# Kernel optimization log

Measured on AMD Instinct MI355X. Metric: run time of the kernel, lower is better.

Reference implementation:

```python
import jax, jax.numpy as jnp
import numpy as np

B, S, D, E, H, TOPK = 4, 2048, 1024, 32, 128, 4

def setup_inputs() -> dict:
    key = jax.random.key(0)
    k1, k2, k3, k4 = jax.random.split(key, 4)
    x = jax.random.normal(k1, (B, S, D), jnp.float32)
    expert_sel = jax.random.normal(k2, (E, D), jnp.float32) * (D ** -0.5)
    keys = jax.random.normal(k3, (E, D, H), jnp.float32) * (D ** -0.5)
    values = jax.random.normal(k4, (E, H, D), jnp.float32) * (H ** -0.5)
    return {"x": x, "expert_sel": expert_sel, "keys": keys, "values": values, "n_heads": TOPK}

def reference(x, expert_sel, keys, values, n_heads):
    # x: [B,S,D]; expert_sel: [E,D]; keys: [E,D,H]; values: [E,H,D]
    Bv, Sv, Dv = x.shape
    Ev = keys.shape[0]
    xf = x.reshape(-1, Dv)                                  # [N,D]
    N = xf.shape[0]
    gate = jax.nn.sigmoid(xf @ expert_sel.T)                # [N,E] sigmoid gating (sigma-MoE)
    vals, idx = jax.lax.top_k(gate, n_heads)                # [N,k] selected experts + gate weights
    # dense per-token-per-expert gate weights; zero for non-selected experts
    g = jnp.zeros((N, Ev), x.dtype).at[jnp.arange(N)[:, None], idx].set(vals)  # [N,E]
    # grouped expert FFN, expressed densely over the (small) expert axis:
    # out = sum_e g[n,e] * relu(x @ keys[e]) @ values[e]
    h = jax.nn.relu(jnp.einsum('nd,edh->enh', xf, keys))    # [E,N,H]
    out = jnp.einsum('enh,ehd->nd', h * g.T[:, :, None], values)  # [N,D]
    return out.reshape(Bv, Sv, Dv)
```

## Files before the change

### kernel.cpp

```cpp
#include <hip/hip_runtime.h>
#include <hip/hip_bf16.h>

#define NTOK 8192
#define DDIM 1024
#define NEXP 32
#define HDIM 128
#define TOPK 4

typedef __attribute__((ext_vector_type(8))) short bf16x8;
typedef __attribute__((ext_vector_type(4))) float f32x4;

typedef unsigned int uint_g __attribute__((address_space(1)));
typedef unsigned int uint_l __attribute__((address_space(3)));

__device__ __forceinline__ void async_cp16(const void* g, void* l) {
    __builtin_amdgcn_global_load_lds((const uint_g*)g, (uint_l*)l, 16, 0, 0);
}

__device__ inline unsigned short f2bf(float f) {
    unsigned int u = __builtin_bit_cast(unsigned int, f);
    unsigned int r = (u + 0x7fffu + ((u >> 16) & 1u)) >> 16;
    return (unsigned short)r;
}
__device__ inline float bf2f(unsigned short s) {
    unsigned int u = ((unsigned int)s) << 16;
    return __builtin_bit_cast(float, u);
}

__global__ __launch_bounds__(256) void prep_weights(
    const float* __restrict__ x,
    const float* __restrict__ keys, const float* __restrict__ values,
    unsigned short* __restrict__ Kb, unsigned short* __restrict__ Vb,
    unsigned short* __restrict__ Xb)
{
    int idx = blockIdx.x * 256 + threadIdx.x;
    unsigned short o[8];
    if (idx < NEXP * 128 * 128) {
        int n = idx & 127, k0 = (idx >> 7) & 127, e = idx >> 14;
        const float* s = keys + ((size_t)e * DDIM + k0 * 8) * HDIM + n;
        #pragma unroll
        for (int j = 0; j < 8; ++j) o[j] = f2bf(s[(size_t)j * HDIM]);
        *(uint4*)&Kb[(size_t)idx * 8] = *(uint4*)o;
    } else if (idx < 2 * NEXP * 128 * 128) {
        idx -= NEXP * 128 * 128;
        int n = idx & 1023, k0 = (idx >> 10) & 15, e = idx >> 14;
        const float* s = values + ((size_t)e * HDIM + k0 * 8) * DDIM + n;
        #pragma unroll
        for (int j = 0; j < 8; ++j) o[j] = f2bf(s[(size_t)j * DDIM]);
        *(uint4*)&Vb[(size_t)idx * 8] = *(uint4*)o;
    } else {
        idx -= 2 * NEXP * 128 * 128;
        const float* s = x + (size_t)idx * 8;
        #pragma unroll
        for (int j = 0; j < 8; ++j) o[j] = f2bf(s[j]);
        *(uint4*)&Xb[(size_t)idx * 8] = *(uint4*)o;
    }
}

__global__ __launch_bounds__(256) void gate_partial(
    const float* __restrict__ x, const float* __restrict__ es,
    float* __restrict__ gpart)
{
    const int n0    = blockIdx.x * 16;
    const int dbase = blockIdx.y * 256;
    const int tid   = threadIdx.x;

    __shared__ float smem[4608];
    float* Xt  = smem;
    float* Est = smem + 64 * 36;

    const int t4  = (tid & 3) * 4;
    const int e4  = ((tid >> 2) & 7) * 4;
    const int rep = tid >> 5;

    const int xr = tid & 15, xc4 = (tid >> 4) * 4;
    const int er = tid & 31, ec8 = (tid >> 5) * 8;

    float acc[4][4] = {};

    for (int dc = dbase; dc < dbase + 256; dc += 64) {
        __syncthreads();
        {
            float4 v = *(const float4*)&x[(size_t)(n0 + xr) * DDIM + dc + xc4];
            Xt[(xc4 + 0) * 36 + xr] = v.x; Xt[(xc4 + 1) * 36 + xr] = v.y;
            Xt[(xc4 + 2) * 36 + xr] = v.z; Xt[(xc4 + 3) * 36 + xr] = v.w;
        }
        #pragma unroll
        for (int i = 0; i < 2; ++i) {
            float4 v = *(const float4*)&es[(size_t)er * DDIM + dc + ec8 + i * 4];
            Est[(ec8 + i * 4 + 0) * 36 + er] = v.x;
            Est[(ec8 + i * 4 + 1) * 36 + er] = v.y;
            Est[(ec8 + i * 4 + 2) * 36 + er] = v.z;
            Est[(ec8 + i * 4 + 3) * 36 + er] = v.w;
        }
        __syncthreads();

        #pragma unroll
        for (int s = 0; s < 8; ++s) {
            int d = s * 8 + rep;
            float4 xv = *(const float4*)&Xt[d * 36 + t4];
            float4 ev = *(const float4*)&Est[d * 36 + e4];
            const float xa[4] = {xv.x, xv.y, xv.z, xv.w};
            const float ea[4] = {ev.x, ev.y, ev.z, ev.w};
            #pragma unroll
            for (int i = 0; i < 4; ++i)
                #pragma unroll
                for (int j = 0; j < 4; ++j)
                    acc[i][j] = fmaf(xa[i], ea[j], acc[i][j]);
        }
    }

    __syncthreads();
    float* Lp = smem;
    #pragma unroll
    for (int i = 0; i < 4; ++i)
        #pragma unroll
        for (int j = 0; j < 4; ++j)
            Lp[(rep * 16 + t4 + i) * 33 + e4 + j] = acc[i][j];
    __syncthreads();

    for (int p = tid; p < 16 * 32; p += 256) {
        int tok = p >> 5, e = p & 31;
        float s = 0.f;
        #pragma unroll
        for (int r = 0; r < 8; ++r) s += Lp[(r * 16 + tok) * 33 + e];
        gpart[((size_t)blockIdx.y * NTOK + n0 + tok) * NEXP + e] = s;
    }
}

__global__ __launch_bounds__(256) void topk_scatter(
    const float* __restrict__ gpart,
    int* __restrict__ cnt, int* __restrict__ tok_list, float* __restrict__ gates)
{
    const int tid = threadIdx.x;
    const int n   = blockIdx.x * 256 + tid;

    __shared__ int hist[NEXP];
    __shared__ int bbase[NEXP];
    if (tid < NEXP) hist[tid] = 0;

    float lg[NEXP];
    #pragma unroll
    for (int i = 0; i < 8; ++i) {
        float4 v = *(const float4*)&gpart[(size_t)n * NEXP + i * 4];
        lg[i*4+0] = v.x; lg[i*4+1] = v.y; lg[i*4+2] = v.z; lg[i*4+3] = v.w;
    }
    #pragma unroll
    for (int j = 1; j < 4; ++j)
        #pragma unroll
        for (int i = 0; i < 8; ++i) {
            float4 v = *(const float4*)&gpart[((size_t)j * NTOK + n) * NEXP + i * 4];
            lg[i*4+0] += v.x; lg[i*4+1] += v.y; lg[i*4+2] += v.z; lg[i*4+3] += v.w;
        }

    int sel[TOPK]; float sv[TOPK];
    #pragma unroll
    for (int j = 0; j < TOPK; ++j) {
        float bv = -3.0e38f; int bi = 0;
        #pragma unroll
        for (int e = 0; e < NEXP; ++e) {
            bool taken = false;
            #pragma unroll
            for (int q = 0; q < j; ++q) taken = taken || (sel[q] == e);
            float v = taken ? -3.0e38f : lg[e];
            if (v > bv) { bv = v; bi = e; }
        }
        sel[j] = bi; sv[j] = bv;
    }

    __syncthreads();
    int lpos[TOPK];
    #pragma unroll
    for (int j = 0; j < TOPK; ++j) {
        gates[n * TOPK + j] = 1.f / (1.f + expf(-sv[j]));
        lpos[j] = atomicAdd(&hist[sel[j]], 1);
    }
    __syncthreads();
    if (tid < NEXP) bbase[tid] = atomicAdd(&cnt[tid], hist[tid]);
    __syncthreads();
    #pragma unroll
    for (int j = 0; j < TOPK; ++j)
        tok_list[(size_t)sel[j] * NTOK + bbase[sel[j]] + lpos[j]] = n * TOPK + j;
}

__global__ __launch_bounds__(256) void ffn_fused(
    const unsigned short* __restrict__ Xb,
    const unsigned short* __restrict__ Kb,
    const unsigned short* __restrict__ Vb,
    const int* __restrict__ cnt, const int* __restrict__ tok_list,
    const float* __restrict__ gates,
    unsigned short* __restrict__ Ob)
{
    const int bid = blockIdx.x;
    const int e = bid & 31, tile = bid >> 5;
    const int c = cnt[e], base = tile * 32;
    if (base >= c) return;
    const int nt   = min(32, c - base);
    const int tid  = threadIdx.x, wave = tid >> 6, lane = tid & 63;
    const int lm   = lane & 15, quad = lane >> 4;
    const int r2   = (wave >> 1) * 16;
    const int c2   = (wave & 1) * 64;
    const int cw   = (wave & 1) * 32;

    __shared__ __align__(16) unsigned short KV[8192];
    __shared__ __align__(16) unsigned short XO[2304];
    __shared__ __align__(16) unsigned short Hs[32 * 136];
    __shared__ int slot[32]; __shared__ int gtok[32]; __shared__ float gs[32];

    if (tid < 32) {
        if (tid < nt) {
            int v = tok_list[(size_t)e * NTOK + base + tid];
            slot[tid] = v; gtok[tid] = v >> 2; gs[tid] = gates[v];
        } else { slot[tid] = -1; gtok[tid] = 0; gs[tid] = 0.f; }
    }
    __syncthreads();

    const unsigned short* Ke   = Kb + (size_t)e * 131072;
    const unsigned short* Ve   = Vb + (size_t)e * 131072;
    const unsigned short* xrow = Xb + (size_t)gtok[lane & 31] * DDIM + (lane >> 5) * 8;

    f32x4 acc[4];
    #pragma unroll
    for (int j = 0; j < 4; ++j) acc[j] = (f32x4){0.f, 0.f, 0.f, 0.f};

    auto stageA = [&](int t) {
        int dc = t * 64;
        #pragma unroll
        for (int i = 0; i < 4; ++i) {
            int p = wave * 4 + i;
            async_cp16(Ke + ((size_t)(dc / 8 + (p >> 1)) * 128 + (p & 1) * 64 + lane) * 8,
                       &KV[p * 512]);
        }
        if (wave == 0) {
            #pragma unroll
            for (int p = 0; p < 4; ++p)
                async_cp16(xrow + dc + p * 16, &XO[p * 512]);
        }
    };

    stageA(0);
    __syncthreads();

    for (int t = 0; t < 16; ++t) {
        #pragma unroll
        for (int ks = 0; ks < 2; ++ks) {
            int k0 = ks * 4 + quad;
            bf16x8 a = *(const bf16x8*)&XO[(k0 * 32 + r2 + lm) * 8];
            #pragma unroll
            for (int tj = 0; tj < 4; ++tj) {
                bf16x8 bb = *(const bf16x8*)&KV[(k0 * 128 + c2 + tj * 16 + lm) * 8];
                acc[tj] = __builtin_amdgcn_mfma_f32_16x16x32_bf16(a, bb, acc[tj], 0, 0, 0);
            }
        }
        if (t < 15) {
            __syncthreads();
            stageA(t + 1);
            __syncthreads();
        }
    }

    #pragma unroll
    for (int reg = 0; reg < 4; ++reg) {
        int m = r2 + quad * 4 + reg;
        float g = gs[m];
        #pragma unroll
        for (int tj = 0; tj < 4; ++tj)
            Hs[m * 136 + c2 + tj * 16 + lm] = f2bf(fmaxf(acc[tj][reg], 0.f) * g);
    }
    __syncthreads();

    auto stageV = [&](int cc) {
        #pragma unroll
        for (int i = 0; i < 4; ++i) {
            int p = wave * 4 + i;
            async_cp16(Ve + ((size_t)p * 1024 + cc * 64 + lane) * 8, &KV[p * 512]);
        }
    };

    stageV(0);
    __syncthreads();

    const int om = tid >> 3, oseg = tid & 7;
    const int os = slot[om];

    for (int cc = 0; cc < 16; ++cc) {
        f32x4 acc2[2];
        acc2[0] = (f32x4){0.f, 0.f, 0.f, 0.f};
        acc2[1] = (f32x4){0.f, 0.f, 0.f, 0.f};

        #pragma unroll
        for (int ks = 0; ks < 4; ++ks) {
            int k0 = ks * 4 + quad;
            bf16x8 a = *(const bf16x8*)&Hs[(r2 + lm) * 136 + k0 * 8];
            #pragma unroll
            for (int tj = 0; tj < 2; ++tj) {
                bf16x8 bb = *(const bf16x8*)&KV[(k0 * 64 + cw + tj * 16 + lm) * 8];
                acc2[tj] = __builtin_amdgcn_mfma_f32_16x16x32_bf16(a, bb, acc2[tj], 0, 0, 0);
            }
        }

        #pragma unroll
        for (int reg = 0; reg < 4; ++reg) {
            int m = r2 + quad * 4 + reg;
            XO[m * 72 + cw + lm]      = f2bf(acc2[0][reg]);
            XO[m * 72 + cw + 16 + lm] = f2bf(acc2[1][reg]);
        }
        __syncthreads();

        if (os >= 0) {
            uint4 v = *(const uint4*)&XO[om * 72 + oseg * 8];
            *(uint4*)&Ob[(size_t)os * DDIM + cc * 64 + oseg * 8] = v;
        }
        if (cc < 15) stageV(cc + 1);
        __syncthreads();
    }
}

__global__ __launch_bounds__(256) void reduce_out(
    const unsigned short* __restrict__ Ob, float* __restrict__ out)
{
    const int tid = threadIdx.x;
    const int n   = blockIdx.x * 2 + (tid >> 7);
    const int cc  = (tid & 127) * 8;

    float s[8] = {};
    #pragma unroll
    for (int j = 0; j < 4; ++j) {
        uint4 v = *(const uint4*)&Ob[((size_t)n * 4 + j) * DDIM + cc];
        const unsigned int w[4] = {v.x, v.y, v.z, v.w};
        #pragma unroll
        for (int q = 0; q < 4; ++q) {
            s[q * 2 + 0] += bf2f((unsigned short)(w[q] & 0xffff));
            s[q * 2 + 1] += bf2f((unsigned short)(w[q] >> 16));
        }
    }
    float4 o0 = {s[0], s[1], s[2], s[3]};
    float4 o1 = {s[4], s[5], s[6], s[7]};
    *(float4*)&out[(size_t)n * DDIM + cc]     = o0;
    *(float4*)&out[(size_t)n * DDIM + cc + 4] = o1;
}

extern "C" void kernel_launch(void* const* d_in, const int* in_sizes, int n_in,
                              void* d_out, int out_size, void* d_ws, size_t ws_size,
                              hipStream_t stream) {
    const float* x      = (const float*)d_in[0];
    const float* es     = (const float*)d_in[1];
    const float* keys   = (const float*)d_in[2];
    const float* values = (const float*)d_in[3];
    float* out          = (float*)d_out;

    char* w = (char*)d_ws;
    int*   cnt      = (int*)w;               w += 256;
    int*   tok_list = (int*)w;               w += (size_t)NEXP * NTOK * sizeof(int);
    float* gates    = (float*)w;             w += (size_t)NTOK * TOPK * sizeof(float);
    float* gpart    = (float*)w;             w += (size_t)4 * NTOK * NEXP * sizeof(float);
    unsigned short* Kb = (unsigned short*)w; w += (size_t)NEXP * 128 * 128 * 8 * 2;
    unsigned short* Vb = (unsigned short*)w; w += (size_t)NEXP * 16 * 1024 * 8 * 2;
    unsigned short* Xb = (unsigned short*)w; w += (size_t)NTOK * DDIM * 2;
    unsigned short* Ob = (unsigned short*)w;

    hipMemsetAsync(cnt, 0, NEXP * sizeof(int), stream);

    prep_weights<<<8192, 256, 0, stream>>>(x, keys, values, Kb, Vb, Xb);
    gate_partial<<<dim3(NTOK / 16, 4), 256, 0, stream>>>(x, es, gpart);
    topk_scatter<<<NTOK / 256, 256, 0, stream>>>(gpart, cnt, tok_list, gates);

    ffn_fused<<<128 * NEXP, 256, 0, stream>>>(Xb, Kb, Vb, cnt, tok_list, gates, Ob);
    reduce_out<<<NTOK / 2, 256, 0, stream>>>(Ob, out);
}
```

Measured before the change: 204.0 us.

## Enlarge per-expert token tile from 32 to 64 rows per block

Each block now handles 64 routed tokens per expert instead of 32, with every wave computing two 16-row MFMA tiles against each loaded key/value fragment. The aim is to halve how often expert key/value weights are re-streamed per token, raising reuse of each LDS-staged weight tile. The token-row loads are spread over all waves, and the output write-back moves two 16-byte chunks per thread. In exchange there are fewer active blocks, more accumulator registers and more shared memory per block. The Hs padding of 140 also breaks 16-byte alignment for the vector LDS reads on odd rows.

```diff
diff --git a/kernel.cpp b/kernel.cpp
--- a/kernel.cpp
+++ b/kernel.cpp
@@ -193,21 +193,21 @@
 {
     const int bid = blockIdx.x;
     const int e = bid & 31, tile = bid >> 5;
-    const int c = cnt[e], base = tile * 32;
+    const int c = cnt[e], base = tile * 64;
     if (base >= c) return;
-    const int nt   = min(32, c - base);
+    const int nt   = min(64, c - base);
     const int tid  = threadIdx.x, wave = tid >> 6, lane = tid & 63;
     const int lm   = lane & 15, quad = lane >> 4;
-    const int r2   = (wave >> 1) * 16;
+    const int r2   = (wave >> 1) * 32;
     const int c2   = (wave & 1) * 64;
     const int cw   = (wave & 1) * 32;
 
     __shared__ __align__(16) unsigned short KV[8192];
-    __shared__ __align__(16) unsigned short XO[2304];
-    __shared__ __align__(16) unsigned short Hs[32 * 136];
-    __shared__ int slot[32]; __shared__ int gtok[32]; __shared__ float gs[32];
-
-    if (tid < 32) {
+    __shared__ __align__(16) unsigned short XO[4608];
+    __shared__ __align__(16) unsigned short Hs[64 * 140];
+    __shared__ int slot[64]; __shared__ int gtok[64]; __shared__ float gs[64];
+
+    if (tid < 64) {
         if (tid < nt) {
             int v = tok_list[(size_t)e * NTOK + base + tid];
             slot[tid] = v; gtok[tid] = v >> 2; gs[tid] = gates[v];
@@ -215,13 +215,15 @@
     }
     __syncthreads();
 
-    const unsigned short* Ke   = Kb + (size_t)e * 131072;
-    const unsigned short* Ve   = Vb + (size_t)e * 131072;
-    const unsigned short* xrow = Xb + (size_t)gtok[lane & 31] * DDIM + (lane >> 5) * 8;
-
-    f32x4 acc[4];
-    #pragma unroll
-    for (int j = 0; j < 4; ++j) acc[j] = (f32x4){0.f, 0.f, 0.f, 0.f};
+    const unsigned short* Ke    = Kb + (size_t)e * 131072;
+    const unsigned short* Ve    = Vb + (size_t)e * 131072;
+    const unsigned short* xrowb = Xb + (size_t)gtok[lane] * DDIM;
+
+    f32x4 acc[2][4];
+    #pragma unroll
+    for (int i = 0; i < 2; ++i)
+        #pragma unroll
+        for (int j = 0; j < 4; ++j) acc[i][j] = (f32x4){0.f, 0.f, 0.f, 0.f};
 
     auto stageA = [&](int t) {
         int dc = t * 64;
@@ -231,10 +233,10 @@
             async_cp16(Ke + ((size_t)(dc / 8 + (p >> 1)) * 128 + (p & 1) * 64 + lane) * 8,
                        &KV[p * 512]);
         }
-        if (wave == 0) {
-            #pragma unroll
-            for (int p = 0; p < 4; ++p)
-                async_cp16(xrow + dc + p * 16, &XO[p * 512]);
+        #pragma unroll
+        for (int i = 0; i < 2; ++i) {
+            int k0 = wave * 2 + i;
+            async_cp16(xrowb + dc + k0 * 8, &XO[k0 * 512]);
         }
     };
 
@@ -245,11 +247,13 @@
         #pragma unroll
         for (int ks = 0; ks < 2; ++ks) {
             int k0 = ks * 4 + quad;
-            bf16x8 a = *(const bf16x8*)&XO[(k0 * 32 + r2 + lm) * 8];
+            bf16x8 a0 = *(const bf16x8*)&XO[(k0 * 64 + r2 + lm) * 8];
+            bf16x8 a1 = *(const bf16x8*)&XO[(k0 * 64 + r2 + 16 + lm) * 8];
             #pragma unroll
             for (int tj = 0; tj < 4; ++tj) {
                 bf16x8 bb = *(const bf16x8*)&KV[(k0 * 128 + c2 + tj * 16 + lm) * 8];
-                acc[tj] = __builtin_amdgcn_mfma_f32_16x16x32_bf16(a, bb, acc[tj], 0, 0, 0);
+                acc[0][tj] = __builtin_amdgcn_mfma_f32_16x16x32_bf16(a0, bb, acc[0][tj], 0, 0, 0);
+                acc[1][tj] = __builtin_amdgcn_mfma_f32_16x16x32_bf16(a1, bb, acc[1][tj], 0, 0, 0);
             }
         }
         if (t < 15) {
@@ -260,13 +264,15 @@
     }
 
     #pragma unroll
-    for (int reg = 0; reg < 4; ++reg) {
-        int m = r2 + quad * 4 + reg;
-        float g = gs[m];
-        #pragma unroll
-        for (int tj = 0; tj < 4; ++tj)
-            Hs[m * 136 + c2 + tj * 16 + lm] = f2bf(fmaxf(acc[tj][reg], 0.f) * g);
-    }
+    for (int ti = 0; ti < 2; ++ti)
+        #pragma unroll
+        for (int reg = 0; reg < 4; ++reg) {
+            int m = r2 + ti * 16 + quad * 4 + reg;
+            float g = gs[m];
+            #pragma unroll
+            for (int tj = 0; tj < 4; ++tj)
+                Hs[m * 140 + c2 + tj * 16 + lm] = f2bf(fmaxf(acc[ti][tj][reg], 0.f) * g);
+        }
     __syncthreads();
 
     auto stageV = [&](int cc) {
@@ -280,36 +286,46 @@
     stageV(0);
     __syncthreads();
 
-    const int om = tid >> 3, oseg = tid & 7;
+    const int om = tid >> 2, oq = tid & 3;
     const int os = slot[om];
 
     for (int cc = 0; cc < 16; ++cc) {
-        f32x4 acc2[2];
-        acc2[0] = (f32x4){0.f, 0.f, 0.f, 0.f};
-        acc2[1] = (f32x4){0.f, 0.f, 0.f, 0.f};
+        f32x4 acc2[2][2];
+        #pragma unroll
+        for (int i = 0; i < 2; ++i) {
+            acc2[i][0] = (f32x4){0.f, 0.f, 0.f, 0.f};
+            acc2[i][1] = (f32x4){0.f, 0.f, 0.f, 0.f};
+        }
 
         #pragma unroll
         for (int ks = 0; ks < 4; ++ks) {
             int k0 = ks * 4 + quad;
-            bf16x8 a = *(const bf16x8*)&Hs[(r2 + lm) * 136 + k0 * 8];
+            bf16x8 a0 = *(const bf16x8*)&Hs[(r2 + lm) * 140 + k0 * 8];
+            bf16x8 a1 = *(const bf16x8*)&Hs[(r2 + 16 + lm) * 140 + k0 * 8];
             #pragma unroll
             for (int tj = 0; tj < 2; ++tj) {
                 bf16x8 bb = *(const bf16x8*)&KV[(k0 * 64 + cw + tj * 16 + lm) * 8];
-                acc2[tj] = __builtin_amdgcn_mfma_f32_16x16x32_bf16(a, bb, acc2[tj], 0, 0, 0);
+                acc2[0][tj] = __builtin_amdgcn_mfma_f32_16x16x32_bf16(a0, bb, acc2[0][tj], 0, 0, 0);
+                acc2[1][tj] = __builtin_amdgcn_mfma_f32_16x16x32_bf16(a1, bb, acc2[1][tj], 0, 0, 0);
             }
         }
 
         #pragma unroll
-        for (int reg = 0; reg < 4; ++reg) {
-            int m = r2 + quad * 4 + reg;
-            XO[m * 72 + cw + lm]      = f2bf(acc2[0][reg]);
-            XO[m * 72 + cw + 16 + lm] = f2bf(acc2[1][reg]);
-        }
+        for (int ti = 0; ti < 2; ++ti)
+            #pragma unroll
+            for (int reg = 0; reg < 4; ++reg) {
+                int m = r2 + ti * 16 + quad * 4 + reg;
+                XO[m * 72 + cw + lm]      = f2bf(acc2[ti][0][reg]);
+                XO[m * 72 + cw + 16 + lm] = f2bf(acc2[ti][1][reg]);
+            }
         __syncthreads();
 
         if (os >= 0) {
-            uint4 v = *(const uint4*)&XO[om * 72 + oseg * 8];
-            *(uint4*)&Ob[(size_t)os * DDIM + cc * 64 + oseg * 8] = v;
+            uint4 v0 = *(const uint4*)&XO[om * 72 + oq * 16];
+            uint4 v1 = *(const uint4*)&XO[om * 72 + oq * 16 + 8];
+            unsigned short* op = Ob + (size_t)os * DDIM + cc * 64 + oq * 16;
+            *(uint4*)op       = v0;
+            *(uint4*)(op + 8) = v1;
         }
         if (cc < 15) stageV(cc + 1);
         __syncthreads();
```

Measured after the change: 201.3 us. About the same (-1.3%).
